# Kernel optimization log

Hardware: AMD Instinct MI355X
Metric: run time of the kernel (lower is better)

## Reference

```python
import jax, jax.numpy as jnp
import numpy as np

B, T, D, H, FF, TB = 4, 512, 768, 12, 3072, 64
DK = D // H
E = float(np.e)
NEG = -1e9  # stand-in for float('-inf') masked_fill; rows always have valid entries


def layer_norm(x, g, b, eps=1e-5):
    m = jnp.mean(x, axis=-1, keepdims=True)
    v = jnp.mean((x - m) ** 2, axis=-1, keepdims=True)
    return (x - m) * jax.lax.rsqrt(v + eps) * g + b


def setup_inputs() -> dict:
    key = jax.random.key(0)
    ks = jax.random.split(key, 20)
    s = 0.02
    w = lambda k, shape: jax.random.normal(k, shape, jnp.float32) * s
    return {
        "x": jax.random.normal(ks[0], (B, T, D), jnp.float32),
        "batch_temporal_mat": jax.random.uniform(ks[1], (B, T, T), jnp.float32, 0.0, 100.0),
        "padding_masks": jnp.ones((B, 1, T, T), jnp.int32),
        # attention linears (stored (in,out): y = x @ W + b, equals torch x @ W_t.T + b)
        "wq": w(ks[2], (D, D)), "bq": w(ks[3], (D,)),
        "wk": w(ks[4], (D, D)), "bk": w(ks[5], (D,)),
        "wv": w(ks[6], (D, D)), "bv": w(ks[7], (D,)),
        "wp": w(ks[8], (D, D)), "bp": w(ks[9], (D,)),
        # temporal-bias MLP: Linear(1,TB) -> leaky_relu(0.2) -> Linear(TB,1)
        "tb1_w": w(ks[10], (1, TB)), "tb1_b": w(ks[11], (TB,)),
        "tb2_w": w(ks[12], (TB, 1)), "tb2_b": w(ks[13], (1,)),
        # FFN
        "fc1_w": w(ks[14], (D, FF)), "fc1_b": w(ks[15], (FF,)),
        "fc2_w": w(ks[16], (FF, D)), "fc2_b": w(ks[17], (D,)),
        # layernorms
        "ln1_g": jnp.ones((D,), jnp.float32), "ln1_b": jnp.zeros((D,), jnp.float32),
        "ln2_g": jnp.ones((D,), jnp.float32), "ln2_b": jnp.zeros((D,), jnp.float32),
    }


def _block(x, batch_temporal_mat, padding_masks,
           wq, bq, wk, bk, wv, bv, wp, bp,
           tb1_w, tb1_b, tb2_w, tb2_b,
           fc1_w, fc1_b, fc2_w, fc2_b,
           ln1_g, ln1_b, ln2_g, ln2_b):
    # pre-LN attention sublayer
    h = layer_norm(x, ln1_g, ln1_b)
    q = (h @ wq + bq).reshape(B, T, H, DK).transpose(0, 2, 1, 3)  # (B,H,T,DK)
    k = (h @ wk + bk).reshape(B, T, H, DK).transpose(0, 2, 1, 3)
    v = (h @ wv + bv).reshape(B, T, H, DK).transpose(0, 2, 1, 3)
    scores = jnp.einsum('bhid,bhjd->bhij', q, k) * (DK ** -0.5)  # (B,H,T,T)

    # temporal bias: 1/log(e + dt), then per-(i,j) MLP with leaky_relu(0.2)
    tm = 1.0 / jnp.log(E + batch_temporal_mat)                    # (B,T,T)
    hb = jax.nn.leaky_relu(tm[..., None] @ tb1_w + tb1_b, 0.2)    # (B,T,T,TB)
    bias = (hb @ tb2_w + tb2_b)[..., 0]                           # (B,T,T)
    scores = scores + bias[:, None]

    # padding mask then causal (future) mask with CLS row 0 fully visible
    scores = jnp.where(padding_masks == 0, NEG, scores)
    causal = jnp.triu(jnp.ones((T, T), bool), 1).at[0, :].set(False)
    scores = jnp.where(causal, NEG, scores)

    p = jax.nn.softmax(scores, axis=-1)
    out = jnp.einsum('bhij,bhjd->bhid', p, v).transpose(0, 2, 1, 3).reshape(B, T, D)
    out = out @ wp + bp
    x = x + out

    # pre-LN FFN sublayer (exact GELU as in nn.GELU default)
    h2 = layer_norm(x, ln2_g, ln2_b)
    m = jax.nn.gelu(h2 @ fc1_w + fc1_b, approximate=False) @ fc2_w + fc2_b
    return x + m


def reference(x, batch_temporal_mat, padding_masks,
              wq, bq, wk, bk, wv, bv, wp, bp,
              tb1_w, tb1_b, tb2_w, tb2_b,
              fc1_w, fc1_b, fc2_w, fc2_b,
              ln1_g, ln1_b, ln2_g, ln2_b):
    return _block(x, batch_temporal_mat, padding_masks,
                  wq, bq, wk, bk, wv, bv, wp, bp,
                  tb1_w, tb1_b, tb2_w, tb2_b,
                  fc1_w, fc1_b, fc2_w, fc2_b,
                  ln1_g, ln1_b, ln2_g, ln2_b)
```

## Files before the change

kernel.cpp:

```cpp
#include <hip/hip_runtime.h>
#include <hip/hip_bf16.h>
#include <math.h>

#define B_ 4
#define T_ 512
#define D_ 768
#define H_ 12
#define FF_ 3072
#define DK_ 64
#define NTOK (B_*T_)
#define NEGV -1e9f

typedef unsigned short u16;
typedef __bf16 bfx8 __attribute__((ext_vector_type(8)));
typedef float f32x4 __attribute__((ext_vector_type(4)));
typedef u16 u16x8 __attribute__((ext_vector_type(8)));

__device__ __forceinline__ u16 f2bf(float f) {
  union { float f; unsigned u; } v; v.f = f;
  unsigned r = (v.u + 0x7FFFu + ((v.u >> 16) & 1u)) >> 16;
  return (u16)r;
}

__device__ __forceinline__ void glds16(const u16* g, u16* l) {
  __builtin_amdgcn_global_load_lds((const __attribute__((address_space(1))) void*)g,
                                   (__attribute__((address_space(3))) void*)l, 16, 0, 0);
}

__global__ __launch_bounds__(256) void prep_kernel(
    const float* __restrict__ x,
    const float* __restrict__ wq, const float* __restrict__ wk,
    const float* __restrict__ wv, const float* __restrict__ wp,
    const float* __restrict__ fc1, const float* __restrict__ fc2,
    u16* wqT, u16* wkT, u16* wvT, u16* wpT, u16* fc1T, u16* fc2T,
    const float* __restrict__ ln1g, const float* __restrict__ ln1b, u16* __restrict__ hbuf,
    const float* __restrict__ tmat, const int* __restrict__ pad,
    const float* __restrict__ tb1w, const float* __restrict__ tb1b,
    const float* __restrict__ tb2w, const float* __restrict__ tb2b,
    float* __restrict__ biasM)
{
  const int bid = blockIdx.x;
  const int tid = threadIdx.x;
  if (bid < 6912) {
    __shared__ float tile[32][33];
    const float* in; u16* outp; int K, N, local;
    if (bid < 2304) {
      int m = bid / 576; local = bid % 576; K = 768; N = 768;
      in   = m == 0 ? wq  : (m == 1 ? wk  : (m == 2 ? wv  : wp));
      outp = m == 0 ? wqT : (m == 1 ? wkT : (m == 2 ? wvT : wpT));
    } else if (bid < 4608) {
      local = bid - 2304; K = 768; N = 3072; in = fc1; outp = fc1T;
    } else {
      local = bid - 4608; K = 3072; N = 768; in = fc2; outp = fc2T;
    }
    const int nt = N / 32;
    const int n0 = (local % nt) * 32, k0 = (local / nt) * 32;
    const int tx = tid & 31, ty = tid >> 5;
    #pragma unroll
    for (int i = 0; i < 4; ++i) {
      int r = ty + i * 8;
      tile[r][tx] = in[(size_t)(k0 + r) * N + n0 + tx];
    }
    __syncthreads();
    #pragma unroll
    for (int i = 0; i < 4; ++i) {
      int r = ty + i * 8;
      outp[(size_t)(n0 + r) * K + k0 + tx] = f2bf(tile[tx][r]);
    }
  } else if (bid < 8960) {
    const int row = bid - 6912;
    const float* xr = x + (size_t)row * D_;
    float v0 = xr[tid], v1 = xr[tid + 256], v2 = xr[tid + 512];
    float s = v0 + v1 + v2;
    float sq = v0 * v0 + v1 * v1 + v2 * v2;
    #pragma unroll
    for (int o = 32; o > 0; o >>= 1) { s += __shfl_down(s, o); sq += __shfl_down(sq, o); }
    __shared__ float ss[4], s2[4];
    int w = tid >> 6;
    if ((tid & 63) == 0) { ss[w] = s; s2[w] = sq; }
    __syncthreads();
    s = ss[0] + ss[1] + ss[2] + ss[3];
    sq = s2[0] + s2[1] + s2[2] + s2[3];
    float mean = s * (1.0f / 768.0f);
    float inv = rsqrtf(sq * (1.0f / 768.0f) - mean * mean + 1e-5f);
    u16* orow = hbuf + (size_t)row * D_;
    orow[tid]       = f2bf((v0 - mean) * inv * ln1g[tid]       + ln1b[tid]);
    orow[tid + 256] = f2bf((v1 - mean) * inv * ln1g[tid + 256] + ln1b[tid + 256]);
    orow[tid + 512] = f2bf((v2 - mean) * inv * ln1g[tid + 512] + ln1b[tid + 512]);
  } else {
    __shared__ float sw1[64], sb1[64], sw2[64];
    if (tid < 64) {
      sw1[tid] = tb1w[tid];
      sb1[tid] = tb1b[tid];
      sw2[tid] = tb2w[tid];
    }
    __syncthreads();
    size_t idx = (size_t)(bid - 8960) * 256 + tid;
    float tm = 1.0f / __logf(2.718281828459045f + tmat[idx]);
    float acc = tb2b[0];
    #pragma unroll
    for (int t = 0; t < 64; ++t) {
      float u = fmaf(tm, sw1[t], sb1[t]);
      u = u > 0.0f ? u : 0.2f * u;
      acc = fmaf(u, sw2[t], acc);
    }
    biasM[idx] = (pad[idx] == 0) ? NEGV : acc;
  }
}

__device__ __forceinline__ void gemm_tile_p2(
    const u16* __restrict__ A, const u16* __restrict__ BT,
    int K, int nk, int m0, int n0, int k0,
    u16* As, u16* Bs, f32x4 acc[4][4])
{
  const int tid = threadIdx.x;
  const int w = tid >> 6, lane = tid & 63;
  const int lr = lane & 15, lk = (lane >> 4) * 8;
  const int wm = (w >> 1) * 64, wn = (w & 1) * 64;
  const int c0 = w * 64 + lane, c1 = 256 + c0;
  const int r0 = c0 >> 2, o0 = (c0 & 3) * 8;
  const int r1 = c1 >> 2, o1 = (c1 & 3) * 8;
  const u16* gA0 = A  + (size_t)(m0 + r0) * K + k0 + o0;
  const u16* gA1 = A  + (size_t)(m0 + r1) * K + k0 + o1;
  const u16* gB0 = BT + (size_t)(n0 + r0) * K + k0 + o0;
  const u16* gB1 = BT + (size_t)(n0 + r1) * K + k0 + o1;
  u16* la0 = As + w * 512;
  u16* la1 = As + 2048 + w * 512;
  u16* lb0 = Bs + w * 512;
  u16* lb1 = Bs + 2048 + w * 512;
#define ISSUE_TILE(kk, b) do { \
    glds16(gA0 + (size_t)(kk) * 32, la0 + (b) * 4096); \
    glds16(gA1 + (size_t)(kk) * 32, la1 + (b) * 4096); \
    glds16(gB0 + (size_t)(kk) * 32, lb0 + (b) * 4096); \
    glds16(gB1 + (size_t)(kk) * 32, lb1 + (b) * 4096); } while (0)
  ISSUE_TILE(0, 0);
  if (nk > 1) ISSUE_TILE(1, 1);
  int cb = 0;
  for (int kt = 0; kt < nk; ++kt) {
    if (kt < nk - 2) asm volatile("s_waitcnt vmcnt(4)" ::: "memory");
    else             asm volatile("s_waitcnt vmcnt(0)" ::: "memory");
    __builtin_amdgcn_sched_barrier(0);
    __builtin_amdgcn_s_barrier();
    __builtin_amdgcn_sched_barrier(0);
    const u16* Asc = As + cb * 4096;
    const u16* Bsc = Bs + cb * 4096;
    bfx8 af[4], bfr[4];
    #pragma unroll
    for (int t = 0; t < 4; ++t) {
      af[t]  = *(const bfx8*)&Asc[(wm + t * 16 + lr) * 32 + lk];
      bfr[t] = *(const bfx8*)&Bsc[(wn + t * 16 + lr) * 32 + lk];
    }
    #pragma unroll
    for (int rt = 0; rt < 4; ++rt)
      #pragma unroll
      for (int ct = 0; ct < 4; ++ct)
        acc[rt][ct] = __builtin_amdgcn_mfma_f32_16x16x32_bf16(af[rt], bfr[ct], acc[rt][ct], 0, 0, 0);
    if (kt + 2 < nk) {
      int nb = cb + 2; if (nb >= 3) nb -= 3;
      ISSUE_TILE(kt + 2, nb);
    }
    cb = cb + 1; if (cb >= 3) cb = 0;
  }
#undef ISSUE_TILE
}

__global__ __launch_bounds__(256) void gemm_qkv(
    const u16* __restrict__ A,
    const u16* __restrict__ wqT, const u16* __restrict__ wkT, const u16* __restrict__ wvT,
    const float* __restrict__ bq, const float* __restrict__ bk, const float* __restrict__ bv,
    u16* __restrict__ qo, u16* __restrict__ ko, u16* __restrict__ vo)
{
  __shared__ u16 As[3 * 128 * 32];
  __shared__ u16 Bs[3 * 128 * 32];
  const int z = blockIdx.z;
  const u16* BT = z == 0 ? wqT : (z == 1 ? wkT : wvT);
  const float* bias = z == 0 ? bq : (z == 1 ? bk : bv);
  u16* outp = z == 0 ? qo : (z == 1 ? ko : vo);
  const float scale = z == 0 ? 0.125f : 1.0f;
  const int m0 = blockIdx.y * 128, n0 = blockIdx.x * 128;
  f32x4 acc[4][4];
  #pragma unroll
  for (int a = 0; a < 4; ++a)
    #pragma unroll
    for (int bb = 0; bb < 4; ++bb) acc[a][bb] = (f32x4){0.f, 0.f, 0.f, 0.f};
  gemm_tile_p2(A, BT, D_, D_ / 32, m0, n0, 0, As, Bs, acc);
  const int tid = threadIdx.x;
  const int w = tid >> 6, lane = tid & 63;
  const int lr = lane & 15;
  const int wm = (w >> 1) * 64, wn = (w & 1) * 64;
  #pragma unroll
  for (int rt = 0; rt < 4; ++rt)
    #pragma unroll
    for (int ct = 0; ct < 4; ++ct)
      #pragma unroll
      for (int r = 0; r < 4; ++r) {
        int m = m0 + wm + rt * 16 + (lane >> 4) * 4 + r;
        int n = n0 + wn + ct * 16 + lr;
        float val = (acc[rt][ct][r] + bias[n]) * scale;
        int b = m >> 9, t = m & 511, hh = n >> 6, d = n & 63;
        if (z < 2) outp[(((size_t)b * H_ + hh) * T_ + t) * DK_ + d] = f2bf(val);
        else       outp[(((size_t)b * H_ + hh) * DK_ + d) * T_ + t] = f2bf(val);
      }
}

__global__ __launch_bounds__(256) void gemm_part(
    const u16* __restrict__ A, const u16* __restrict__ BT,
    float* __restrict__ part, int M, int N, int K, int Ksplit)
{
  __shared__ u16 As[3 * 128 * 32];
  __shared__ u16 Bs[3 * 128 * 32];
  const int m0 = blockIdx.y * 128, n0 = blockIdx.x * 128;
  const int kz = blockIdx.z;
  f32x4 acc[4][4];
  #pragma unroll
  for (int a = 0; a < 4; ++a)
    #pragma unroll
    for (int bb = 0; bb < 4; ++bb) acc[a][bb] = (f32x4){0.f, 0.f, 0.f, 0.f};
  gemm_tile_p2(A, BT, K, Ksplit / 32, m0, n0, kz * Ksplit, As, Bs, acc);
  const int tid = threadIdx.x;
  const int w = tid >> 6, lane = tid & 63;
  const int lr = lane & 15;
  const int wm = (w >> 1) * 64, wn = (w & 1) * 64;
  float* pp = part + (size_t)kz * M * N;
  #pragma unroll
  for (int rt = 0; rt < 4; ++rt)
    #pragma unroll
    for (int ct = 0; ct < 4; ++ct)
      #pragma unroll
      for (int r = 0; r < 4; ++r) {
        int m = m0 + wm + rt * 16 + (lane >> 4) * 4 + r;
        int n = n0 + wn + ct * 16 + lr;
        pp[(size_t)m * N + n] = acc[rt][ct][r];
      }
}

__global__ __launch_bounds__(256) void gemm_gelu(
    const u16* __restrict__ A, const u16* __restrict__ BT,
    const float* __restrict__ bias, u16* __restrict__ outp, int M, int N, int K)
{
  __shared__ u16 As[3 * 128 * 32];
  __shared__ u16 Bs[3 * 128 * 32];
  const int m0 = blockIdx.y * 128, n0 = blockIdx.x * 128;
  f32x4 acc[4][4];
  #pragma unroll
  for (int a = 0; a < 4; ++a)
    #pragma unroll
    for (int bb = 0; bb < 4; ++bb) acc[a][bb] = (f32x4){0.f, 0.f, 0.f, 0.f};
  gemm_tile_p2(A, BT, K, K / 32, m0, n0, 0, As, Bs, acc);
  const int tid = threadIdx.x;
  const int w = tid >> 6, lane = tid & 63;
  const int lr = lane & 15;
  const int wm = (w >> 1) * 64, wn = (w & 1) * 64;
  #pragma unroll
  for (int rt = 0; rt < 4; ++rt)
    #pragma unroll
    for (int ct = 0; ct < 4; ++ct)
      #pragma unroll
      for (int r = 0; r < 4; ++r) {
        int m = m0 + wm + rt * 16 + (lane >> 4) * 4 + r;
        int n = n0 + wn + ct * 16 + lr;
        float val = acc[rt][ct][r] + bias[n];
        float gl = 0.5f * val * (1.0f + erff(val * 0.7071067811865475f));
        outp[(size_t)m * N + n] = f2bf(gl);
      }
}

__global__ __launch_bounds__(256) void reduce_ln(
    const float* __restrict__ part, const float* __restrict__ x, const float* __restrict__ bp,
    const float* __restrict__ g, const float* __restrict__ bta,
    float* __restrict__ x1, u16* __restrict__ h2)
{
  const int row = blockIdx.x;
  const int tid = threadIdx.x;
  const size_t base = (size_t)row * D_;
  const size_t slab = (size_t)NTOK * D_;
  float v[3];
  float s = 0.f, sq = 0.f;
  #pragma unroll
  for (int i = 0; i < 3; ++i) {
    int c = tid + i * 256;
    float val = x[base + c] + bp[c] + part[base + c] + part[slab + base + c];
    v[i] = val;
    s += val; sq += val * val;
  }
  #pragma unroll
  for (int o = 32; o > 0; o >>= 1) { s += __shfl_down(s, o); sq += __shfl_down(sq, o); }
  __shared__ float ss[4], s2[4];
  int w = tid >> 6;
  if ((tid & 63) == 0) { ss[w] = s; s2[w] = sq; }
  __syncthreads();
  s = ss[0] + ss[1] + ss[2] + ss[3];
  sq = s2[0] + s2[1] + s2[2] + s2[3];
  float mean = s * (1.0f / 768.0f);
  float inv = rsqrtf(sq * (1.0f / 768.0f) - mean * mean + 1e-5f);
  #pragma unroll
  for (int i = 0; i < 3; ++i) {
    int c = tid + i * 256;
    x1[base + c] = v[i];
    h2[base + c] = f2bf((v[i] - mean) * inv * g[c] + bta[c]);
  }
}

__global__ __launch_bounds__(256) void reduce_out(
    const float* __restrict__ part, const float* __restrict__ x1,
    const float* __restrict__ bias, float* __restrict__ out)
{
  const size_t i = (size_t)blockIdx.x * 256 + threadIdx.x;
  const size_t slab = (size_t)NTOK * D_ / 4;
  float4 b = ((const float4*)bias)[i % (D_ / 4)];
  float4 a = ((const float4*)x1)[i];
  float4 p0 = ((const float4*)part)[i];
  float4 p1 = ((const float4*)part)[i + slab];
  float4 p2 = ((const float4*)part)[i + 2 * slab];
  float4 p3 = ((const float4*)part)[i + 3 * slab];
  float4 o;
  o.x = a.x + b.x + p0.x + p1.x + p2.x + p3.x;
  o.y = a.y + b.y + p0.y + p1.y + p2.y + p3.y;
  o.z = a.z + b.z + p0.z + p1.z + p2.z + p3.z;
  o.w = a.w + b.w + p0.w + p1.w + p2.w + p3.w;
  ((float4*)out)[i] = o;
}

__global__ __launch_bounds__(256) void attn_kernel(
    const u16* __restrict__ q, const u16* __restrict__ k, const u16* __restrict__ vT,
    const float* __restrict__ biasM, u16* __restrict__ ao)
{
  __shared__ u16 P[32 * 512];
  __shared__ float pmax[128], psum[128];
  const int tid = threadIdx.x;
  const int w = tid >> 6, lane = tid & 63;
  const int lr = lane & 15, hi = lane >> 4, lk = hi * 8;

  const int bid = blockIdx.x;
  const int xcd = bid & 7, idx = bid >> 3;
  const int bh = xcd * 6 + (idx >> 4);
  const int i0 = (idx & 15) * 32;
  const int b = bh / H_, h = bh % H_;
  const int tmax = (i0 == 0) ? 31 : ((i0 >> 4) + 1);
  const int nks  = (i0 == 0) ? 16 : ((i0 >> 5) + 1);

  bfx8 qf[2][2];
  #pragma unroll
  for (int g = 0; g < 2; ++g)
    #pragma unroll
    for (int ks = 0; ks < 2; ++ks)
      qf[g][ks] = *(const bfx8*)(q + ((size_t)bh * T_ + i0 + g * 16 + lr) * DK_ + ks * 32 + lk);
  f32x4 acc[8][2];
  float mx[2][4];
  #pragma unroll
  for (int g = 0; g < 2; ++g)
    #pragma unroll
    for (int r = 0; r < 4; ++r) mx[g][r] = -3.4e38f;
  #pragma unroll
  for (int ct = 0; ct < 8; ++ct) {
    const int t = ct * 4 + w;
    if (t > tmax) continue;
    const int j0 = t * 16;
    bfx8 kf0 = *(const bfx8*)(k + ((size_t)bh * T_ + j0 + lr) * DK_ + lk);
    bfx8 kf1 = *(const bfx8*)(k + ((size_t)bh * T_ + j0 + lr) * DK_ + 32 + lk);
    const int j = j0 + lr;
    #pragma unroll
    for (int g = 0; g < 2; ++g) {
      f32x4 a0 = (f32x4){0.f, 0.f, 0.f, 0.f};
      a0 = __builtin_amdgcn_mfma_f32_16x16x32_bf16(qf[g][0], kf0, a0, 0, 0, 0);
      a0 = __builtin_amdgcn_mfma_f32_16x16x32_bf16(qf[g][1], kf1, a0, 0, 0, 0);
      #pragma unroll
      for (int r = 0; r < 4; ++r) {
        int i = i0 + g * 16 + hi * 4 + r;
        float s = a0[r] + biasM[((size_t)b * T_ + i) * T_ + j];
        if (j > i && i != 0) s = NEGV;
        a0[r] = s;
        mx[g][r] = fmaxf(mx[g][r], s);
      }
      acc[ct][g] = a0;
    }
  }
  #pragma unroll
  for (int o = 1; o < 16; o <<= 1)
    #pragma unroll
    for (int g = 0; g < 2; ++g)
      #pragma unroll
      for (int r = 0; r < 4; ++r) mx[g][r] = fmaxf(mx[g][r], __shfl_xor(mx[g][r], o));
  if (lr == 0) {
    #pragma unroll
    for (int g = 0; g < 2; ++g)
      #pragma unroll
      for (int r = 0; r < 4; ++r) pmax[w * 32 + g * 16 + hi * 4 + r] = mx[g][r];
  }
  __syncthreads();

  float M2[2][4], sm[2][4];
  #pragma unroll
  for (int g = 0; g < 2; ++g)
    #pragma unroll
    for (int r = 0; r < 4; ++r) {
      int row = g * 16 + hi * 4 + r;
      M2[g][r] = fmaxf(fmaxf(pmax[row], pmax[32 + row]), fmaxf(pmax[64 + row], pmax[96 + row]));
      sm[g][r] = 0.f;
    }
  char* Pb = (char*)P;
  #pragma unroll
  for (int ct = 0; ct < 8; ++ct) {
    const int t = ct * 4 + w;
    if (t > tmax) continue;
    const int col = t * 16 + lr;
    #pragma unroll
    for (int g = 0; g < 2; ++g)
      #pragma unroll
      for (int r = 0; r < 4; ++r) {
        float pexp = __expf(acc[ct][g][r] - M2[g][r]);
        sm[g][r] += pexp;
        int row = g * 16 + hi * 4 + r;
        int byte = (row * 1024 + col * 2) ^ ((row & 7) << 4);
        *(u16*)(Pb + byte) = f2bf(pexp);
      }
  }
  #pragma unroll
  for (int o = 1; o < 16; o <<= 1)
    #pragma unroll
    for (int g = 0; g < 2; ++g)
      #pragma unroll
      for (int r = 0; r < 4; ++r) sm[g][r] += __shfl_xor(sm[g][r], o);
  if (lr == 0) {
    #pragma unroll
    for (int g = 0; g < 2; ++g)
      #pragma unroll
      for (int r = 0; r < 4; ++r) psum[w * 32 + g * 16 + hi * 4 + r] = sm[g][r];
  }
  __syncthreads();

  float rinv[2][4];
  #pragma unroll
  for (int g = 0; g < 2; ++g)
    #pragma unroll
    for (int r = 0; r < 4; ++r) {
      int row = g * 16 + hi * 4 + r;
      rinv[g][r] = 1.0f / (psum[row] + psum[32 + row] + psum[64 + row] + psum[96 + row]);
    }

  {
    const int n0 = w * 16;
    f32x4 oa0 = (f32x4){0.f, 0.f, 0.f, 0.f};
    f32x4 oa1 = (f32x4){0.f, 0.f, 0.f, 0.f};
    for (int ks = 0; ks < nks; ++ks) {
      bfx8 vf = *(const bfx8*)(vT + ((size_t)bh * DK_ + n0 + lr) * T_ + ks * 32 + lk);
      int byte0 = (lr * 1024 + (ks * 32 + lk) * 2) ^ ((lr & 7) << 4);
      int byte1 = ((16 + lr) * 1024 + (ks * 32 + lk) * 2) ^ ((lr & 7) << 4);
      bfx8 pa0 = *(const bfx8*)(Pb + byte0);
      bfx8 pa1 = *(const bfx8*)(Pb + byte1);
      oa0 = __builtin_amdgcn_mfma_f32_16x16x32_bf16(pa0, vf, oa0, 0, 0, 0);
      oa1 = __builtin_amdgcn_mfma_f32_16x16x32_bf16(pa1, vf, oa1, 0, 0, 0);
    }
    #pragma unroll
    for (int r = 0; r < 4; ++r) {
      int i = i0 + hi * 4 + r;
      ao[((size_t)b * T_ + i) * D_ + h * DK_ + n0 + lr] = f2bf(oa0[r] * rinv[0][r]);
    }
    #pragma unroll
    for (int r = 0; r < 4; ++r) {
      int i = i0 + 16 + hi * 4 + r;
      ao[((size_t)b * T_ + i) * D_ + h * DK_ + n0 + lr] = f2bf(oa1[r] * rinv[1][r]);
    }
  }
}

extern "C" void kernel_launch(void* const* d_in, const int* in_sizes, int n_in,
                              void* d_out, int out_size, void* d_ws, size_t ws_size,
                              hipStream_t stream) {
  (void)in_sizes; (void)n_in; (void)out_size; (void)ws_size;
  const float* x    = (const float*)d_in[0];
  const float* tmat = (const float*)d_in[1];
  const int*   pad  = (const int*)d_in[2];
  const float* wq = (const float*)d_in[3];  const float* bq = (const float*)d_in[4];
  const float* wk = (const float*)d_in[5];  const float* bk = (const float*)d_in[6];
  const float* wv = (const float*)d_in[7];  const float* bv = (const float*)d_in[8];
  const float* wp = (const float*)d_in[9];  const float* bp = (const float*)d_in[10];
  const float* tb1w = (const float*)d_in[11]; const float* tb1b = (const float*)d_in[12];
  const float* tb2w = (const float*)d_in[13]; const float* tb2b = (const float*)d_in[14];
  const float* fc1w = (const float*)d_in[15]; const float* fc1b = (const float*)d_in[16];
  const float* fc2w = (const float*)d_in[17]; const float* fc2b = (const float*)d_in[18];
  const float* ln1g = (const float*)d_in[19]; const float* ln1b = (const float*)d_in[20];
  const float* ln2g = (const float*)d_in[21]; const float* ln2b = (const float*)d_in[22];
  float* out = (float*)d_out;

  char* p = (char*)d_ws;
  u16* wqT  = (u16*)p; p += (size_t)768 * 768 * 2;
  u16* wkT  = (u16*)p; p += (size_t)768 * 768 * 2;
  u16* wvT  = (u16*)p; p += (size_t)768 * 768 * 2;
  u16* wpT  = (u16*)p; p += (size_t)768 * 768 * 2;
  u16* fc1T = (u16*)p; p += (size_t)768 * 3072 * 2;
  u16* fc2T = (u16*)p; p += (size_t)3072 * 768 * 2;
  float* x1 = (float*)p; p += (size_t)NTOK * D_ * 4;
  u16* gbuf = (u16*)p; p += (size_t)NTOK * FF_ * 2;
  char* pool = p;
  u16*   hbuf  = (u16*)(pool + 0);
  u16*   qb    = (u16*)(pool + 3145728);
  u16*   kb    = (u16*)(pool + 6291456);
  u16*   vTb   = (u16*)(pool + 9437184);
  float* biasM = (float*)(pool + 12582912);
  u16*   ao    = (u16*)(pool + 16777216);
  u16*   h2    = (u16*)(pool + 19922944);
  float* partP = (float*)(pool + 0);
  float* partF = (float*)(pool + 0);

  prep_kernel<<<13056, 256, 0, stream>>>(x, wq, wk, wv, wp, fc1w, fc2w,
                                         wqT, wkT, wvT, wpT, fc1T, fc2T,
                                         ln1g, ln1b, hbuf,
                                         tmat, pad, tb1w, tb1b, tb2w, tb2b, biasM);

  gemm_qkv<<<dim3(6, 16, 3), 256, 0, stream>>>(hbuf, wqT, wkT, wvT, bq, bk, bv, qb, kb, vTb);
  attn_kernel<<<768, 256, 0, stream>>>(qb, kb, vTb, biasM, ao);

  gemm_part<<<dim3(6, 16, 2), 256, 0, stream>>>(ao, wpT, partP, NTOK, 768, 768, 384);
  reduce_ln<<<NTOK, 256, 0, stream>>>(partP, x, bp, ln2g, ln2b, x1, h2);

  gemm_gelu<<<dim3(24, 16), 256, 0, stream>>>(h2, fc1T, fc1b, gbuf, NTOK, FF_, 768);

  gemm_part<<<dim3(6, 16, 4), 256, 0, stream>>>(gbuf, fc2T, partF, NTOK, 768, 3072, 768);
  reduce_out<<<NTOK * D_ / 4 / 256, 256, 0, stream>>>(partF, x1, fc2b, out);
}
```

Before: 139.4 us.

## Replace split-K partial buffers and reductions with atomicAdd into pre-initialized outputs

The split-K GEMMs now atomically add their partial sums straight into destination buffers. Those buffers are pre-initialized with the residual plus bias: x1 in the LN1 prep step, out in the LN2 kernel. This drops the separate reduce_out kernel and the fp32 partial-slab writes and reads, and the workspace pool aliasing is replaced by dedicated buffers. The cost is fp32 atomics on every output element, and summation order becomes nondeterministic.

```diff
diff --git a/kernel.cpp b/kernel.cpp
--- a/kernel.cpp
+++ b/kernel.cpp
@@ -34,6 +34,7 @@
     const float* __restrict__ fc1, const float* __restrict__ fc2,
     u16* wqT, u16* wkT, u16* wvT, u16* wpT, u16* fc1T, u16* fc2T,
     const float* __restrict__ ln1g, const float* __restrict__ ln1b, u16* __restrict__ hbuf,
+    const float* __restrict__ bp, float* __restrict__ x1,
     const float* __restrict__ tmat, const int* __restrict__ pad,
     const float* __restrict__ tb1w, const float* __restrict__ tb1b,
     const float* __restrict__ tb2w, const float* __restrict__ tb2b,
@@ -84,9 +85,13 @@
     float mean = s * (1.0f / 768.0f);
     float inv = rsqrtf(sq * (1.0f / 768.0f) - mean * mean + 1e-5f);
     u16* orow = hbuf + (size_t)row * D_;
+    float* x1r = x1 + (size_t)row * D_;
     orow[tid]       = f2bf((v0 - mean) * inv * ln1g[tid]       + ln1b[tid]);
     orow[tid + 256] = f2bf((v1 - mean) * inv * ln1g[tid + 256] + ln1b[tid + 256]);
     orow[tid + 512] = f2bf((v2 - mean) * inv * ln1g[tid + 512] + ln1b[tid + 512]);
+    x1r[tid]       = v0 + bp[tid];
+    x1r[tid + 256] = v1 + bp[tid + 256];
+    x1r[tid + 512] = v2 + bp[tid + 512];
   } else {
     __shared__ float sw1[64], sb1[64], sw2[64];
     if (tid < 64) {
@@ -203,9 +208,9 @@
       }
 }
 
-__global__ __launch_bounds__(256) void gemm_part(
+__global__ __launch_bounds__(256) void gemm_atomic(
     const u16* __restrict__ A, const u16* __restrict__ BT,
-    float* __restrict__ part, int M, int N, int K, int Ksplit)
+    float* __restrict__ dst, int M, int N, int K, int Ksplit)
 {
   __shared__ u16 As[3 * 128 * 32];
   __shared__ u16 Bs[3 * 128 * 32];
@@ -221,7 +226,6 @@
   const int w = tid >> 6, lane = tid & 63;
   const int lr = lane & 15;
   const int wm = (w >> 1) * 64, wn = (w & 1) * 64;
-  float* pp = part + (size_t)kz * M * N;
   #pragma unroll
   for (int rt = 0; rt < 4; ++rt)
     #pragma unroll
@@ -230,7 +234,7 @@
       for (int r = 0; r < 4; ++r) {
         int m = m0 + wm + rt * 16 + (lane >> 4) * 4 + r;
         int n = n0 + wn + ct * 16 + lr;
-        pp[(size_t)m * N + n] = acc[rt][ct][r];
+        atomicAdd(&dst[(size_t)m * N + n], acc[rt][ct][r]);
       }
 }
 
@@ -265,21 +269,19 @@
       }
 }
 
-__global__ __launch_bounds__(256) void reduce_ln(
-    const float* __restrict__ part, const float* __restrict__ x, const float* __restrict__ bp,
-    const float* __restrict__ g, const float* __restrict__ bta,
-    float* __restrict__ x1, u16* __restrict__ h2)
+__global__ __launch_bounds__(256) void ln2_kernel(
+    const float* __restrict__ x1, const float* __restrict__ g, const float* __restrict__ bta,
+    const float* __restrict__ fc2b, u16* __restrict__ h2, float* __restrict__ outInit)
 {
   const int row = blockIdx.x;
   const int tid = threadIdx.x;
   const size_t base = (size_t)row * D_;
-  const size_t slab = (size_t)NTOK * D_;
   float v[3];
   float s = 0.f, sq = 0.f;
   #pragma unroll
   for (int i = 0; i < 3; ++i) {
     int c = tid + i * 256;
-    float val = x[base + c] + bp[c] + part[base + c] + part[slab + base + c];
+    float val = x1[base + c];
     v[i] = val;
     s += val; sq += val * val;
   }
@@ -296,29 +298,9 @@
   #pragma unroll
   for (int i = 0; i < 3; ++i) {
     int c = tid + i * 256;
-    x1[base + c] = v[i];
     h2[base + c] = f2bf((v[i] - mean) * inv * g[c] + bta[c]);
-  }
-}
-
-__global__ __launch_bounds__(256) void reduce_out(
-    const float* __restrict__ part, const float* __restrict__ x1,
-    const float* __restrict__ bias, float* __restrict__ out)
-{
-  const size_t i = (size_t)blockIdx.x * 256 + threadIdx.x;
-  const size_t slab = (size_t)NTOK * D_ / 4;
-  float4 b = ((const float4*)bias)[i % (D_ / 4)];
-  float4 a = ((const float4*)x1)[i];
-  float4 p0 = ((const float4*)part)[i];
-  float4 p1 = ((const float4*)part)[i + slab];
-  float4 p2 = ((const float4*)part)[i + 2 * slab];
-  float4 p3 = ((const float4*)part)[i + 3 * slab];
-  float4 o;
-  o.x = a.x + b.x + p0.x + p1.x + p2.x + p3.x;
-  o.y = a.y + b.y + p0.y + p1.y + p2.y + p3.y;
-  o.z = a.z + b.z + p0.z + p1.z + p2.z + p3.z;
-  o.w = a.w + b.w + p0.w + p1.w + p2.w + p3.w;
-  ((float4*)out)[i] = o;
+    outInit[base + c] = v[i] + fc2b[c];
+  }
 }
 
 __global__ __launch_bounds__(256) void attn_kernel(
@@ -492,30 +474,26 @@
   u16* fc2T = (u16*)p; p += (size_t)3072 * 768 * 2;
   float* x1 = (float*)p; p += (size_t)NTOK * D_ * 4;
   u16* gbuf = (u16*)p; p += (size_t)NTOK * FF_ * 2;
-  char* pool = p;
-  u16*   hbuf  = (u16*)(pool + 0);
-  u16*   qb    = (u16*)(pool + 3145728);
-  u16*   kb    = (u16*)(pool + 6291456);
-  u16*   vTb   = (u16*)(pool + 9437184);
-  float* biasM = (float*)(pool + 12582912);
-  u16*   ao    = (u16*)(pool + 16777216);
-  u16*   h2    = (u16*)(pool + 19922944);
-  float* partP = (float*)(pool + 0);
-  float* partF = (float*)(pool + 0);
+  u16* hbuf = (u16*)p; p += (size_t)NTOK * D_ * 2;
+  u16* qb   = (u16*)p; p += (size_t)NTOK * D_ * 2;
+  u16* kb   = (u16*)p; p += (size_t)NTOK * D_ * 2;
+  u16* vTb  = (u16*)p; p += (size_t)NTOK * D_ * 2;
+  float* biasM = (float*)p; p += (size_t)B_ * T_ * T_ * 4;
+  u16* ao   = (u16*)p; p += (size_t)NTOK * D_ * 2;
+  u16* h2   = (u16*)p; p += (size_t)NTOK * D_ * 2;
 
   prep_kernel<<<13056, 256, 0, stream>>>(x, wq, wk, wv, wp, fc1w, fc2w,
                                          wqT, wkT, wvT, wpT, fc1T, fc2T,
-                                         ln1g, ln1b, hbuf,
+                                         ln1g, ln1b, hbuf, bp, x1,
                                          tmat, pad, tb1w, tb1b, tb2w, tb2b, biasM);
 
   gemm_qkv<<<dim3(6, 16, 3), 256, 0, stream>>>(hbuf, wqT, wkT, wvT, bq, bk, bv, qb, kb, vTb);
   attn_kernel<<<768, 256, 0, stream>>>(qb, kb, vTb, biasM, ao);
 
-  gemm_part<<<dim3(6, 16, 2), 256, 0, stream>>>(ao, wpT, partP, NTOK, 768, 768, 384);
-  reduce_ln<<<NTOK, 256, 0, stream>>>(partP, x, bp, ln2g, ln2b, x1, h2);
+  gemm_atomic<<<dim3(6, 16, 2), 256, 0, stream>>>(ao, wpT, x1, NTOK, 768, 768, 384);
+  ln2_kernel<<<NTOK, 256, 0, stream>>>(x1, ln2g, ln2b, fc2b, h2, out);
 
   gemm_gelu<<<dim3(24, 16), 256, 0, stream>>>(h2, fc1T, fc1b, gbuf, NTOK, FF_, 768);
 
-  gemm_part<<<dim3(6, 16, 4), 256, 0, stream>>>(gbuf, fc2T, partF, NTOK, 768, 3072, 768);
-  reduce_out<<<NTOK * D_ / 4 / 256, 256, 0, stream>>>(partF, x1, fc2b, out);
-}
+  gemm_atomic<<<dim3(6, 16, 4), 256, 0, stream>>>(gbuf, fc2T, out, NTOK, 768, 3072, 768);
+}
```

Result: slower. 148.5 us (+6.5%).
